# Performance work log

Hardware: AMD Instinct MI355X
Metric: run time of the kernel (lower is better)

The kernel has to match this reference:

```python
import jax, jax.numpy as jnp
import numpy as np

NUM_EMBEDDINGS = 8192
EMBED_DIM = 64
NUM_BATCH = 4
N_VOX = 32768
EPS = 1e-10


def setup_inputs() -> dict:
    key = jax.random.key(0)
    k1, k2, k3, k4 = jax.random.split(key, 4)
    z_feats = jax.random.normal(k1, (N_VOX, EMBED_DIM), dtype=jnp.float32)
    batch_ids = jax.random.randint(k2, (N_VOX, 1), 0, NUM_BATCH)
    xyz = jax.random.randint(k3, (N_VOX, 3), 0, 64)
    z_coords = jnp.concatenate([batch_ids, xyz], axis=1).astype(jnp.int32)
    codebook = jax.random.normal(k4, (NUM_EMBEDDINGS, EMBED_DIM), dtype=jnp.float32)
    return {"z_feats": z_feats, "z_coords": z_coords, "codebook": codebook}


def reference(z_feats, z_coords, codebook):
    # squared euclidean distances [N, K]; argmin identical to torch.cdist argmin
    d2 = (jnp.sum(z_feats * z_feats, axis=1, keepdims=True)
          - 2.0 * (z_feats @ codebook.T)
          + jnp.sum(codebook * codebook, axis=1)[None, :])
    encoding_indices = jnp.argmin(d2, axis=1)              # [N]
    quantized = codebook[encoding_indices]                 # [N, D] gather

    # losses (gradient mode, use_ema_update=False)
    commitment_loss = jnp.mean((z_feats - jax.lax.stop_gradient(quantized)) ** 2)
    vq_loss = jnp.mean((quantized - jax.lax.stop_gradient(z_feats)) ** 2)

    # straight-through estimator
    quantized_st = z_feats + jax.lax.stop_gradient(quantized - z_feats)

    # per-sample codebook stats (vectorized over the batch dimension)
    batch_ids = z_coords[:, 0]
    counts = jnp.zeros((NUM_BATCH, NUM_EMBEDDINGS), jnp.float32).at[batch_ids, encoding_indices].add(1.0)
    per_sample_n = jnp.sum(counts, axis=1, keepdims=True)  # tokens per sample
    probs = counts / per_sample_n
    sample_entropy = -jnp.sum(probs * jnp.log(probs + EPS), axis=1)  # [B]
    avg_entropy = jnp.mean(sample_entropy)
    avg_perplexity = jnp.mean(jnp.exp(sample_entropy))
    avg_unique_count = jnp.mean(jnp.sum(counts > 0, axis=1).astype(jnp.float32))
    utilization_ratio = avg_unique_count / NUM_EMBEDDINGS * 100.0

    encoding_indices_st = encoding_indices.astype(jnp.float32)[:, None]
    return (quantized_st, vq_loss, commitment_loss, encoding_indices_st,
            avg_perplexity, avg_entropy, avg_unique_count, utilization_ratio)
```

## Files before the change

kernel.cpp:

```cpp
#include <hip/hip_runtime.h>
#include <math.h>

#define NUM_EMB 8192
#define DIM     64
#define NBATCH  4
#define NVOX    32768
#define TPB     256
#define NSPLIT  8
#define EPB     (NUM_EMB / NSPLIT)
#define CHUNK   64
#define CERT_EPS 0.015f
#define RCH     512

#define OFF_Q     0
#define OFF_VQ    2097152
#define OFF_COMM  2097153
#define OFF_IDX   2097154
#define OFF_PERP  2129922
#define OFF_ENT   2129923
#define OFF_UNIQ  2129924
#define OFF_UTIL  2129925

typedef __bf16 bf16x8 __attribute__((ext_vector_type(8)));
typedef float  f32x4  __attribute__((ext_vector_type(4)));

__device__ __forceinline__ unsigned short f2bf(float f) {
    unsigned u = __float_as_uint(f);
    unsigned r = u + 0x7FFFu + ((u >> 16) & 1u);
    return (unsigned short)(r >> 16);
}
__device__ __forceinline__ float bf2f(unsigned short h) {
    return __uint_as_float(((unsigned)h) << 16);
}
__device__ __forceinline__ unsigned fmap(float f) {
    unsigned u = __float_as_uint(f);
    return (u & 0x80000000u) ? ~u : (u | 0x80000000u);
}

__global__ void prep_kernel(const float* __restrict__ cb,
                            unsigned short* __restrict__ cbh,
                            unsigned short* __restrict__ cbm,
                            float* __restrict__ cnp4,
                            unsigned* __restrict__ counts,
                            unsigned* __restrict__ misc,
                            unsigned long long* __restrict__ merge) {
    int row = blockIdx.x * 4 + (threadIdx.x >> 6);
    int l   = threadIdx.x & 63;
    float f = cb[row * DIM + l];
    unsigned short hh = f2bf(f); float r1 = f - bf2f(hh);
    cbh[row * DIM + l] = hh;
    cbm[row * DIM + l] = f2bf(r1);
    float s = f * f;
#pragma unroll
    for (int o = 32; o > 0; o >>= 1) s += __shfl_xor(s, o, 64);
    if (l < 4) cnp4[row * 4 + l] = -0.5f * s;

    int gid = blockIdx.x * TPB + threadIdx.x;
    if (gid < NBATCH * NUM_EMB) counts[gid] = 0;
    if (gid >= 32768 && gid < 65536) merge[gid - 32768] = ~0ull;
    if (gid < 16) misc[gid] = 0;
}

__global__ __launch_bounds__(TPB) void argmin_kernel(
        const float* __restrict__ z,
        const unsigned short* __restrict__ cbh,
        const unsigned short* __restrict__ cbm,
        const float* __restrict__ cnp4,
        float4* __restrict__ res) {
    __shared__ __align__(16) char lds[2 * CHUNK * 128 + CHUNK * 16];

    const int t  = threadIdx.x;
    const int l  = t & 63, w = t >> 6;
    const int lc = l & 15, lg = l >> 4;
    const int vb = blockIdx.x >> 3, qh = blockIdx.x & 7;
    const int ebase = qh * EPB;

    union U { bf16x8 v; unsigned short s[8]; };
    U Ah[2][2], Am[2][2];
#pragma unroll
    for (int set = 0; set < 2; ++set) {
        const float* zp = z + (size_t)(vb * 128 + w * 32 + set * 16 + lc) * DIM + lg * 8;
#pragma unroll
        for (int ks = 0; ks < 2; ++ks)
#pragma unroll
            for (int j = 0; j < 8; ++j) {
                float f = zp[ks * 32 + j];
                unsigned short hh = f2bf(f);
                Ah[set][ks].s[j] = hh;
                Am[set][ks].s[j] = f2bf(f - bf2f(hh));
            }
    }

    float m1[2][4], m2[2][4]; int ix[2][4];
#pragma unroll
    for (int set = 0; set < 2; ++set)
#pragma unroll
        for (int r = 0; r < 4; ++r) {
            m1[set][r] = -INFINITY; m2[set][r] = -INFINITY; ix[set][r] = 0;
        }

    const int b0 = (lc * 128 + lg * 16) ^ ((lc & 7) << 4);
    const int b1 = b0 ^ 64;
    const int cb0 = 2 * CHUNK * 128 + lc * 16;

    for (int ch = 0; ch < EPB / CHUNK; ++ch) {
        const char* sh = (const char*)cbh + (size_t)(ebase + ch * CHUNK) * 128;
        const char* sm = (const char*)cbm + (size_t)(ebase + ch * CHUNK) * 128;
#pragma unroll
        for (int j = 0; j < 2; ++j) {
            int off = (j * 256 + t) * 16;
            int swz = off ^ (((off >> 7) & 7) << 4);
            *(uint4*)(lds + swz) = *(const uint4*)(sh + off);
            *(uint4*)(lds + CHUNK * 128 + swz) = *(const uint4*)(sm + off);
        }
        if (t < CHUNK)
            ((float4*)(lds + 2 * CHUNK * 128))[t] =
                ((const float4*)cnp4)[ebase + ch * CHUNK + t];
        __syncthreads();

        int e0 = ebase + ch * CHUNK + lc;
#pragma unroll
        for (int tile = 0; tile < CHUNK / 16; ++tile) {
            bf16x8 bh0 = *(const bf16x8*)(lds + b0 + tile * 2048);
            bf16x8 bh1 = *(const bf16x8*)(lds + b1 + tile * 2048);
            bf16x8 bm0 = *(const bf16x8*)(lds + CHUNK * 128 + b0 + tile * 2048);
            bf16x8 bm1 = *(const bf16x8*)(lds + CHUNK * 128 + b1 + tile * 2048);
            f32x4  c0  = *(const f32x4*)(lds + cb0 + tile * 256);
            int eidx = e0 + tile * 16;
#pragma unroll
            for (int set = 0; set < 2; ++set) {
                f32x4 a = c0;
                a = __builtin_amdgcn_mfma_f32_16x16x32_bf16(Ah[set][0].v, bh0, a, 0, 0, 0);
                a = __builtin_amdgcn_mfma_f32_16x16x32_bf16(Am[set][0].v, bh0, a, 0, 0, 0);
                a = __builtin_amdgcn_mfma_f32_16x16x32_bf16(Ah[set][0].v, bm0, a, 0, 0, 0);
                a = __builtin_amdgcn_mfma_f32_16x16x32_bf16(Ah[set][1].v, bh1, a, 0, 0, 0);
                a = __builtin_amdgcn_mfma_f32_16x16x32_bf16(Am[set][1].v, bh1, a, 0, 0, 0);
                a = __builtin_amdgcn_mfma_f32_16x16x32_bf16(Ah[set][1].v, bm1, a, 0, 0, 0);
#pragma unroll
                for (int r = 0; r < 4; ++r) {
                    float v = a[r];
                    m2[set][r] = __builtin_amdgcn_fmed3f(v, m1[set][r], m2[set][r]);
                    if (v > m1[set][r]) { m1[set][r] = v; ix[set][r] = eidx; }
                }
            }
        }
        __syncthreads();
    }

#pragma unroll
    for (int set = 0; set < 2; ++set)
#pragma unroll
        for (int r = 0; r < 4; ++r) {
            float v1 = m1[set][r], v2 = m2[set][r]; int i1 = ix[set][r];
#pragma unroll
            for (int st = 1; st < 16; st <<= 1) {
                float o1 = __shfl_xor(v1, st, 16);
                float o2 = __shfl_xor(v2, st, 16);
                int   oi = __shfl_xor(i1, st, 16);
                float mn = fminf(v1, o1);
                v2 = fmaxf(fmaxf(v2, o2), mn);
                if (o1 > v1 || (o1 == v1 && oi < i1)) { v1 = o1; i1 = oi; }
            }
            if (lc == 0) {
                int vox = vb * 128 + w * 32 + set * 16 + lg * 4 + r;
                res[(size_t)qh * NVOX + vox] =
                    make_float4(v1, v2, __int_as_float(i1), 0.f);
            }
        }
}

__global__ void combine_kernel(const float4* __restrict__ res, float* __restrict__ out) {
    int vox = blockIdx.x * blockDim.x + threadIdx.x;
    float v1 = -INFINITY, v2 = -INFINITY; int idx = 0;
#pragma unroll
    for (int h = 0; h < NSPLIT; ++h) {
        float4 t4 = res[(size_t)h * NVOX + vox];
        float a1 = t4.x, a2 = t4.y; int ai = __float_as_int(t4.z);
        float mn = fminf(v1, a1);
        v2 = fmaxf(fmaxf(v2, a2), mn);
        if (a1 > v1) { v1 = a1; idx = ai; }
    }
    unsigned flag = (v1 - v2 < CERT_EPS) ? 0x80000000u : 0u;
    ((unsigned*)out)[OFF_IDX + vox] = (unsigned)idx | flag;
    if (vox == 0) {
        out[OFF_VQ] = 0.f; out[OFF_COMM] = 0.f; out[OFF_PERP] = 0.f;
        out[OFF_ENT] = 0.f; out[OFF_UNIQ] = 0.f; out[OFF_UTIL] = 0.f;
    }
}

__global__ void gather_kernel(const float* __restrict__ z, const int* __restrict__ zc,
        const float* __restrict__ cb, float* __restrict__ out,
        unsigned* __restrict__ counts, float* __restrict__ sqsum,
        unsigned* __restrict__ list, unsigned* __restrict__ lcount) {
    int vox = blockIdx.x * blockDim.x + threadIdx.x;
    unsigned pk = ((unsigned*)out)[OFF_IDX + vox];
    float s = 0.f;
    if (pk & 0x80000000u) {
        unsigned pos = atomicAdd(lcount, 1u);
        list[pos] = vox;
    } else {
        unsigned idx = pk;
        const float4* crow = (const float4*)(cb + (size_t)idx * DIM);
        const float4* zrow = (const float4*)(z + (size_t)vox * DIM);
        float4* qrow = (float4*)(out + OFF_Q + (size_t)vox * DIM);
#pragma unroll
        for (int i = 0; i < DIM / 4; ++i) {
            float4 c4 = crow[i];
            float4 z4 = zrow[i];
            float dx = z4.x - c4.x, dy = z4.y - c4.y;
            float dz = z4.z - c4.z, dw = z4.w - c4.w;
            s += dx * dx + dy * dy + dz * dz + dw * dw;
            qrow[i] = c4;
        }
        out[OFF_IDX + vox] = (float)idx;
        atomicAdd(&counts[zc[vox * 4] * NUM_EMB + idx], 1u);
    }
#pragma unroll
    for (int o = 32; o > 0; o >>= 1) s += __shfl_down(s, o, 64);
    __shared__ float red[TPB / 64];
    if ((threadIdx.x & 63) == 0) red[threadIdx.x >> 6] = s;
    __syncthreads();
    if (threadIdx.x == 0)
        atomicAdd(sqsum, red[0] + red[1] + red[2] + red[3]);
}

__global__ void repair_scan_kernel(const float* __restrict__ z,
        const float* __restrict__ cb, const unsigned* __restrict__ list,
        const unsigned* __restrict__ lcount,
        unsigned long long* __restrict__ merge) {
    int wid = (blockIdx.x * blockDim.x + threadIdx.x) >> 6;
    int l   = threadIdx.x & 63;
    int nw  = (gridDim.x * blockDim.x) >> 6;
    int nitems = (int)*lcount * (NUM_EMB / RCH);
    int sub = l & 15, ent = l >> 4;

    for (int it = wid; it < nitems; it += nw) {
        int k    = it / (NUM_EMB / RCH);
        int base = (it % (NUM_EMB / RCH)) * RCH;
        int vox  = list[k];
        float4 z4 = ((const float4*)(z + (size_t)vox * DIM))[sub];
        float m = INFINITY; int mi = 0;

        for (int g0 = 0; g0 < RCH / 4; g0 += 4) {
            float d[4];
#pragma unroll
            for (int u = 0; u < 4; ++u) {
                int e = base + (g0 + u) * 4 + ent;
                float4 c4 = ((const float4*)(cb + (size_t)e * DIM))[sub];
                float dx = z4.x - c4.x, dy = z4.y - c4.y;
                float dz = z4.z - c4.z, dw = z4.w - c4.w;
                d[u] = fmaf(dx, dx, fmaf(dy, dy, fmaf(dz, dz, dw * dw)));
            }
#pragma unroll
            for (int st = 1; st < 16; st <<= 1)
#pragma unroll
                for (int u = 0; u < 4; ++u) d[u] += __shfl_xor(d[u], st, 16);
#pragma unroll
            for (int u = 0; u < 4; ++u) {
                int e = base + (g0 + u) * 4 + ent;
                if (d[u] < m) { m = d[u]; mi = e; }
            }
        }
#pragma unroll
        for (int st = 32; st > 0; st >>= 1) {
            float om = __shfl_xor(m, st, 64);
            int   oi = __shfl_xor(mi, st, 64);
            if (om < m || (om == m && oi < mi)) { m = om; mi = oi; }
        }
        if (l == 0) {
            unsigned long long key =
                ((unsigned long long)fmap(m) << 32) | (unsigned)mi;
            atomicMin(&merge[vox], key);
        }
    }
}

__global__ void repair_apply_kernel(const float* __restrict__ z,
        const int* __restrict__ zc, const float* __restrict__ cb,
        const unsigned* __restrict__ list, const unsigned* __restrict__ lcount,
        const unsigned long long* __restrict__ merge, float* __restrict__ out,
        unsigned* __restrict__ counts, float* __restrict__ sqsum) {
    int wid = (blockIdx.x * blockDim.x + threadIdx.x) >> 6;
    int l   = threadIdx.x & 63;
    int n   = (int)*lcount;
    int nw  = (gridDim.x * blockDim.x) >> 6;
    for (int k = wid; k < n; k += nw) {
        int vox = list[k];
        int mi  = (int)(merge[vox] & 0xFFFFFFFFull);
        float cv = cb[(size_t)mi * DIM + l];
        float zv = z[(size_t)vox * DIM + l];
        out[OFF_Q + (size_t)vox * DIM + l] = cv;
        float df = zv - cv;
        float s = df * df;
#pragma unroll
        for (int st = 32; st > 0; st >>= 1) s += __shfl_xor(s, st, 64);
        if (l == 0) {
            out[OFF_IDX + vox] = (float)mi;
            atomicAdd(&counts[zc[vox * 4] * NUM_EMB + mi], 1u);
            atomicAdd(sqsum, s);
        }
    }
}

__global__ void stats_final_kernel(const unsigned* __restrict__ counts,
                                   const float* __restrict__ sqsum,
                                   float* __restrict__ out) {
    int b = blockIdx.x;
    const unsigned* c = counts + b * NUM_EMB;

    __shared__ float sred[TPB / 64];
    float nf = 0.f;
    for (int i = threadIdx.x; i < NUM_EMB; i += TPB) nf += (float)c[i];
#pragma unroll
    for (int o = 32; o > 0; o >>= 1) nf += __shfl_down(nf, o, 64);
    if ((threadIdx.x & 63) == 0) sred[threadIdx.x >> 6] = nf;
    __syncthreads();
    float n = sred[0] + sred[1] + sred[2] + sred[3];
    __syncthreads();

    float ent = 0.f, uniq = 0.f;
    for (int i = threadIdx.x; i < NUM_EMB; i += TPB) {
        unsigned ci = c[i];
        if (ci) {
            float p = (float)ci / n;
            ent -= p * logf(p + 1e-10f);
            uniq += 1.f;
        }
    }
#pragma unroll
    for (int o = 32; o > 0; o >>= 1) {
        ent  += __shfl_down(ent, o, 64);
        uniq += __shfl_down(uniq, o, 64);
    }
    __shared__ float e4[TPB / 64], u4[TPB / 64];
    if ((threadIdx.x & 63) == 0) { e4[threadIdx.x >> 6] = ent; u4[threadIdx.x >> 6] = uniq; }
    __syncthreads();
    if (threadIdx.x == 0) {
        float eb = e4[0] + e4[1] + e4[2] + e4[3];
        float ub = u4[0] + u4[1] + u4[2] + u4[3];
        atomicAdd(&out[OFF_ENT],  eb * 0.25f);
        atomicAdd(&out[OFF_PERP], expf(eb) * 0.25f);
        atomicAdd(&out[OFF_UNIQ], ub * 0.25f);
        atomicAdd(&out[OFF_UTIL], ub * (100.f / (4.f * NUM_EMB)));
        if (b == 0) {
            float loss = *sqsum / (float)((size_t)NVOX * DIM);
            out[OFF_VQ]   = loss;
            out[OFF_COMM] = loss;
        }
    }
}

extern "C" void kernel_launch(void* const* d_in, const int* in_sizes, int n_in,
                              void* d_out, int out_size, void* d_ws, size_t ws_size,
                              hipStream_t stream) {
    const float* z  = (const float*)d_in[0];
    const int*   zc = (const int*)d_in[1];
    const float* cb = (const float*)d_in[2];
    float* out = (float*)d_out;
    char* ws = (char*)d_ws;

    unsigned short* cbh = (unsigned short*)out;
    unsigned short* cbm = cbh + NUM_EMB * DIM;
    float4* res = (float4*)(out + 524288);

    unsigned* counts = (unsigned*)ws;
    unsigned* list   = (unsigned*)(ws + 131072);
    unsigned* misc   = (unsigned*)(ws + 262144);
    unsigned* lcount = misc;
    float*    sqsum  = (float*)(ws + 262148);
    float*    cnp4   = (float*)(ws + 262208);
    unsigned long long* merge = (unsigned long long*)(ws + 393280);

    prep_kernel<<<NUM_EMB / 4, TPB, 0, stream>>>(cb, cbh, cbm, cnp4,
                                                 counts, misc, merge);
    argmin_kernel<<<(NVOX / 128) * NSPLIT, TPB, 0, stream>>>(z, cbh, cbm, cnp4, res);
    combine_kernel<<<NVOX / TPB, TPB, 0, stream>>>(res, out);
    gather_kernel<<<NVOX / TPB, TPB, 0, stream>>>(z, zc, cb, out, counts, sqsum,
                                                  list, lcount);
    repair_scan_kernel<<<512, TPB, 0, stream>>>(z, cb, list, lcount, merge);
    repair_apply_kernel<<<64, TPB, 0, stream>>>(z, zc, cb, list, lcount, merge,
                                                out, counts, sqsum);
    stats_final_kernel<<<NBATCH, TPB, 0, stream>>>(counts, sqsum, out);
}
```

Before: 204.5 us.

## Double-buffer codebook chunks, halve split count, fuse combine into gather

```diff
diff --git a/kernel.cpp b/kernel.cpp
--- a/kernel.cpp
+++ b/kernel.cpp
@@ -6,9 +6,11 @@
 #define NBATCH  4
 #define NVOX    32768
 #define TPB     256
-#define NSPLIT  8
+#define NSPLIT  4
 #define EPB     (NUM_EMB / NSPLIT)
 #define CHUNK   64
+#define NCH     (EPB / CHUNK)
+#define BUFSZ   (CHUNK * 128 * 2 + CHUNK * 4)
 #define CERT_EPS 0.015f
 #define RCH     512
 
@@ -40,10 +42,11 @@
 __global__ void prep_kernel(const float* __restrict__ cb,
                             unsigned short* __restrict__ cbh,
                             unsigned short* __restrict__ cbm,
-                            float* __restrict__ cnp4,
+                            float* __restrict__ cnn,
                             unsigned* __restrict__ counts,
                             unsigned* __restrict__ misc,
-                            unsigned long long* __restrict__ merge) {
+                            unsigned long long* __restrict__ merge,
+                            float* __restrict__ out) {
     int row = blockIdx.x * 4 + (threadIdx.x >> 6);
     int l   = threadIdx.x & 63;
     float f = cb[row * DIM + l];
@@ -53,26 +56,32 @@
     float s = f * f;
 #pragma unroll
     for (int o = 32; o > 0; o >>= 1) s += __shfl_xor(s, o, 64);
-    if (l < 4) cnp4[row * 4 + l] = -0.5f * s;
+    if (l == 0) cnn[row] = -0.5f * s;
 
     int gid = blockIdx.x * TPB + threadIdx.x;
     if (gid < NBATCH * NUM_EMB) counts[gid] = 0;
     if (gid >= 32768 && gid < 65536) merge[gid - 32768] = ~0ull;
     if (gid < 16) misc[gid] = 0;
-}
-
-__global__ __launch_bounds__(TPB) void argmin_kernel(
+    if (blockIdx.x == 0) {
+        if (threadIdx.x < 2) out[OFF_VQ + threadIdx.x] = 0.f;
+        if (threadIdx.x < 4) out[OFF_PERP + threadIdx.x] = 0.f;
+    }
+}
+
+__global__ __launch_bounds__(TPB)
+__attribute__((amdgpu_waves_per_eu(4, 4)))
+void argmin_kernel(
         const float* __restrict__ z,
         const unsigned short* __restrict__ cbh,
         const unsigned short* __restrict__ cbm,
-        const float* __restrict__ cnp4,
+        const float* __restrict__ cnn,
         float4* __restrict__ res) {
-    __shared__ __align__(16) char lds[2 * CHUNK * 128 + CHUNK * 16];
+    __shared__ __align__(16) char lds[2 * BUFSZ];
 
     const int t  = threadIdx.x;
     const int l  = t & 63, w = t >> 6;
     const int lc = l & 15, lg = l >> 4;
-    const int vb = blockIdx.x >> 3, qh = blockIdx.x & 7;
+    const int vb = blockIdx.x >> 2, qh = blockIdx.x & 3;
     const int ebase = qh * EPB;
 
     union U { bf16x8 v; unsigned short s[8]; };
@@ -101,31 +110,41 @@
 
     const int b0 = (lc * 128 + lg * 16) ^ ((lc & 7) << 4);
     const int b1 = b0 ^ 64;
-    const int cb0 = 2 * CHUNK * 128 + lc * 16;
-
-    for (int ch = 0; ch < EPB / CHUNK; ++ch) {
-        const char* sh = (const char*)cbh + (size_t)(ebase + ch * CHUNK) * 128;
-        const char* sm = (const char*)cbm + (size_t)(ebase + ch * CHUNK) * 128;
-#pragma unroll
-        for (int j = 0; j < 2; ++j) {
-            int off = (j * 256 + t) * 16;
-            int swz = off ^ (((off >> 7) & 7) << 4);
-            *(uint4*)(lds + swz) = *(const uint4*)(sh + off);
-            *(uint4*)(lds + CHUNK * 128 + swz) = *(const uint4*)(sm + off);
-        }
-        if (t < CHUNK)
-            ((float4*)(lds + 2 * CHUNK * 128))[t] =
-                ((const float4*)cnp4)[ebase + ch * CHUNK + t];
-        __syncthreads();
+
+    uint4 rh0, rh1, rm0, rm1; float rc;
+#define STAGE_LOAD(CH) {                                                      \
+        const uint4* sh = (const uint4*)(cbh + (size_t)(ebase + (CH) * CHUNK) * DIM); \
+        const uint4* sm = (const uint4*)(cbm + (size_t)(ebase + (CH) * CHUNK) * DIM); \
+        rh0 = sh[t]; rh1 = sh[t + 256];                                       \
+        rm0 = sm[t]; rm1 = sm[t + 256];                                       \
+        if (t < CHUNK) rc = cnn[ebase + (CH) * CHUNK + t];                    \
+    }
+#define STAGE_WRITE(BUF) {                                                    \
+        int o0 = t * 16, o1 = (256 + t) * 16;                                 \
+        int s0 = o0 ^ (((o0 >> 7) & 7) << 4);                                 \
+        int s1 = o1 ^ (((o1 >> 7) & 7) << 4);                                 \
+        *(uint4*)((BUF) + s0) = rh0;  *(uint4*)((BUF) + s1) = rh1;            \
+        *(uint4*)((BUF) + 8192 + s0) = rm0; *(uint4*)((BUF) + 8192 + s1) = rm1; \
+        if (t < CHUNK) ((float*)((BUF) + 16384))[t] = rc;                     \
+    }
+
+    STAGE_LOAD(0);
+    STAGE_WRITE(lds);
+    __syncthreads();
+
+    for (int ch = 0; ch < NCH; ++ch) {
+        char* cur = lds + (ch & 1) * BUFSZ;
+        if (ch + 1 < NCH) STAGE_LOAD(ch + 1);
 
         int e0 = ebase + ch * CHUNK + lc;
 #pragma unroll
         for (int tile = 0; tile < CHUNK / 16; ++tile) {
-            bf16x8 bh0 = *(const bf16x8*)(lds + b0 + tile * 2048);
-            bf16x8 bh1 = *(const bf16x8*)(lds + b1 + tile * 2048);
-            bf16x8 bm0 = *(const bf16x8*)(lds + CHUNK * 128 + b0 + tile * 2048);
-            bf16x8 bm1 = *(const bf16x8*)(lds + CHUNK * 128 + b1 + tile * 2048);
-            f32x4  c0  = *(const f32x4*)(lds + cb0 + tile * 256);
+            bf16x8 bh0 = *(const bf16x8*)(cur + b0 + tile * 2048);
+            bf16x8 bh1 = *(const bf16x8*)(cur + b1 + tile * 2048);
+            bf16x8 bm0 = *(const bf16x8*)(cur + 8192 + b0 + tile * 2048);
+            bf16x8 bm1 = *(const bf16x8*)(cur + 8192 + b1 + tile * 2048);
+            float  cnv = *(const float*)(cur + 16384 + (tile * 16 + lc) * 4);
+            f32x4 c0 = {cnv, cnv, cnv, cnv};
             int eidx = e0 + tile * 16;
 #pragma unroll
             for (int set = 0; set < 2; ++set) {
@@ -145,6 +164,10 @@
             }
         }
         __syncthreads();
+        if (ch + 1 < NCH) {
+            STAGE_WRITE(lds + ((ch + 1) & 1) * BUFSZ);
+            __syncthreads();
+        }
     }
 
 #pragma unroll
@@ -182,10 +205,6 @@
     }
     unsigned flag = (v1 - v2 < CERT_EPS) ? 0x80000000u : 0u;
     ((unsigned*)out)[OFF_IDX + vox] = (unsigned)idx | flag;
-    if (vox == 0) {
-        out[OFF_VQ] = 0.f; out[OFF_COMM] = 0.f; out[OFF_PERP] = 0.f;
-        out[OFF_ENT] = 0.f; out[OFF_UNIQ] = 0.f; out[OFF_UTIL] = 0.f;
-    }
 }
 
 __global__ void gather_kernel(const float* __restrict__ z, const int* __restrict__ zc,
@@ -200,6 +219,50 @@
         list[pos] = vox;
     } else {
         unsigned idx = pk;
+        const float4* crow = (const float4*)(cb + (size_t)idx * DIM);
+        const float4* zrow = (const float4*)(z + (size_t)vox * DIM);
+        float4* qrow = (float4*)(out + OFF_Q + (size_t)vox * DIM);
+#pragma unroll
+        for (int i = 0; i < DIM / 4; ++i) {
+            float4 c4 = crow[i];
+            float4 z4 = zrow[i];
+            float dx = z4.x - c4.x, dy = z4.y - c4.y;
+            float dz = z4.z - c4.z, dw = z4.w - c4.w;
+            s += dx * dx + dy * dy + dz * dz + dw * dw;
+            qrow[i] = c4;
+        }
+        out[OFF_IDX + vox] = (float)idx;
+        atomicAdd(&counts[zc[vox * 4] * NUM_EMB + idx], 1u);
+    }
+#pragma unroll
+    for (int o = 32; o > 0; o >>= 1) s += __shfl_down(s, o, 64);
+    __shared__ float red[TPB / 64];
+    if ((threadIdx.x & 63) == 0) red[threadIdx.x >> 6] = s;
+    __syncthreads();
+    if (threadIdx.x == 0)
+        atomicAdd(sqsum, red[0] + red[1] + red[2] + red[3]);
+}
+
+__global__ void gatherF_kernel(const float* __restrict__ z, const int* __restrict__ zc,
+        const float* __restrict__ cb, const float4* __restrict__ res,
+        float* __restrict__ out, unsigned* __restrict__ counts,
+        float* __restrict__ sqsum, unsigned* __restrict__ list,
+        unsigned* __restrict__ lcount) {
+    int vox = blockIdx.x * blockDim.x + threadIdx.x;
+    float v1 = -INFINITY, v2 = -INFINITY; int idx = 0;
+#pragma unroll
+    for (int h = 0; h < NSPLIT; ++h) {
+        float4 t4 = res[(size_t)h * NVOX + vox];
+        float a1 = t4.x, a2 = t4.y; int ai = __float_as_int(t4.z);
+        float mn = fminf(v1, a1);
+        v2 = fmaxf(fmaxf(v2, a2), mn);
+        if (a1 > v1) { v1 = a1; idx = ai; }
+    }
+    float s = 0.f;
+    if (v1 - v2 < CERT_EPS) {
+        unsigned pos = atomicAdd(lcount, 1u);
+        list[pos] = vox;
+    } else {
         const float4* crow = (const float4*)(cb + (size_t)idx * DIM);
         const float4* zrow = (const float4*)(z + (size_t)vox * DIM);
         float4* qrow = (float4*)(out + OFF_Q + (size_t)vox * DIM);
@@ -361,22 +424,30 @@
 
     unsigned short* cbh = (unsigned short*)out;
     unsigned short* cbm = cbh + NUM_EMB * DIM;
-    float4* res = (float4*)(out + 524288);
 
     unsigned* counts = (unsigned*)ws;
     unsigned* list   = (unsigned*)(ws + 131072);
     unsigned* misc   = (unsigned*)(ws + 262144);
     unsigned* lcount = misc;
     float*    sqsum  = (float*)(ws + 262148);
-    float*    cnp4   = (float*)(ws + 262208);
-    unsigned long long* merge = (unsigned long long*)(ws + 393280);
-
-    prep_kernel<<<NUM_EMB / 4, TPB, 0, stream>>>(cb, cbh, cbm, cnp4,
-                                                 counts, misc, merge);
-    argmin_kernel<<<(NVOX / 128) * NSPLIT, TPB, 0, stream>>>(z, cbh, cbm, cnp4, res);
-    combine_kernel<<<NVOX / TPB, TPB, 0, stream>>>(res, out);
-    gather_kernel<<<NVOX / TPB, TPB, 0, stream>>>(z, zc, cb, out, counts, sqsum,
-                                                  list, lcount);
+    float*    cnn    = (float*)(ws + 262208);
+    unsigned long long* merge = (unsigned long long*)(ws + 294976);
+    size_t res_ws_off = 557120;
+    bool bigws = ws_size >= res_ws_off + (size_t)NSPLIT * NVOX * 16;
+    float4* res = bigws ? (float4*)(ws + res_ws_off)
+                        : (float4*)(out + 524288);
+
+    prep_kernel<<<NUM_EMB / 4, TPB, 0, stream>>>(cb, cbh, cbm, cnn,
+                                                 counts, misc, merge, out);
+    argmin_kernel<<<(NVOX / 128) * NSPLIT, TPB, 0, stream>>>(z, cbh, cbm, cnn, res);
+    if (bigws) {
+        gatherF_kernel<<<NVOX / TPB, TPB, 0, stream>>>(z, zc, cb, res, out,
+                                                       counts, sqsum, list, lcount);
+    } else {
+        combine_kernel<<<NVOX / TPB, TPB, 0, stream>>>(res, out);
+        gather_kernel<<<NVOX / TPB, TPB, 0, stream>>>(z, zc, cb, out, counts,
+                                                      sqsum, list, lcount);
+    }
     repair_scan_kernel<<<512, TPB, 0, stream>>>(z, cb, list, lcount, merge);
     repair_apply_kernel<<<64, TPB, 0, stream>>>(z, zc, cb, list, lcount, merge,
                                                 out, counts, sqsum);
```

Measured after the change: 217.6 us. 6.4% more time.
